# Performance work log

Hardware: AMD Instinct MI355X
Metric: run time of the kernel (lower is better)

The kernel has to match this reference:

```python
import jax, jax.numpy as jnp
import numpy as np

B, L, C, H, MAX_K, TAU = 64, 512, 256, 8, 512, 1.0
N = B * L
DH = C // H


def setup_inputs() -> dict:
    key = jax.random.key(0)
    ks = jax.random.split(key, 16)
    s = 0.02
    return {
        "x": jax.random.normal(ks[0], (N, C), jnp.float32),
        "edge_index": jax.random.randint(ks[1], (2, 200000), 0, N, jnp.int64),
        "batch": jnp.repeat(jnp.arange(B, dtype=jnp.int64), L),
        "token_ratio": jax.random.uniform(ks[2], (B,), jnp.float32, 0.05, 0.95),
        # gumbel = -log(Exp(1)) matches -empty.exponential_().log()
        "gumbel": -jnp.log(jax.random.exponential(ks[3], (B, L), jnp.float32)),
        # scorer: Linear(C,C) -> ReLU -> Linear(C,1)
        "Ws1": jax.random.normal(ks[4], (C, C), jnp.float32) * s,
        "bs1": jnp.zeros((C,), jnp.float32),
        "Ws2": jax.random.normal(ks[5], (1, C), jnp.float32) * s,
        "bs2": jnp.zeros((1,), jnp.float32),
        # MultiheadAttention packed in-proj [3C, C] and out-proj [C, C]
        "Win": jax.random.normal(ks[6], (3 * C, C), jnp.float32) * s,
        "b_in": jnp.zeros((3 * C,), jnp.float32),
        "Wout": jax.random.normal(ks[7], (C, C), jnp.float32) * s,
        "bout": jnp.zeros((C,), jnp.float32),
        # MLP: Linear(C, 2C) -> ReLU -> Linear(2C, C)
        "Wm1": jax.random.normal(ks[8], (2 * C, C), jnp.float32) * s,
        "bm1": jnp.zeros((2 * C,), jnp.float32),
        "Wm2": jax.random.normal(ks[9], (C, 2 * C), jnp.float32) * s,
        "bm2": jnp.zeros((C,), jnp.float32),
    }


def reference(x, edge_index, batch, token_ratio, gumbel,
              Ws1, bs1, Ws2, bs2, Win, b_in, Wout, bout, Wm1, bm1, Wm2, bm2):
    # conv=None, norm=None, eval mode (dropout = identity), equal-length graphs
    h_dense = x.reshape(B, L, C)                                  # to_dense_batch
    real_len = L                                                  # all graphs full
    k_per = jnp.clip(jnp.ceil(token_ratio * real_len).astype(jnp.int32),
                     1, min(MAX_K, L))                            # [B]
    k_max = int(np.max(np.asarray(k_per)))                        # concrete

    # scorer -> log-softmax scores (mask is all True, no -inf fill needed)
    s1 = jax.nn.relu(h_dense @ Ws1.T + bs1)
    scores = (s1 @ Ws2.T + bs2)[..., 0]                           # [B, L]
    log_scores = jax.nn.log_softmax(scores, axis=-1)

    # gumbel top-k with straight-through one-hot mask
    y_soft = jax.nn.softmax((log_scores + gumbel) / TAU, axis=-1)
    _, idx_g = jax.lax.top_k(y_soft, k_max)                       # [B, k_max]
    bidx = jnp.arange(B)[:, None]
    y_hard = jnp.zeros_like(y_soft).at[bidx, idx_g].set(1.0)
    token_mask = y_hard + y_soft - jax.lax.stop_gradient(y_soft)  # == y_hard numerically

    # sort descending, zero tokens beyond k_per[i], scatter back to node order
    sort_idx = jnp.argsort(-jax.lax.stop_gradient(token_mask), axis=-1, stable=True)
    sorted_mask = jnp.take_along_axis(token_mask, sort_idx, axis=1)
    keep = jnp.arange(L)[None, :] < k_per[:, None]
    sorted_mask = jnp.where(keep, sorted_mask, 0.0)
    refined = jnp.zeros_like(sorted_mask).at[bidx, sort_idx].set(sorted_mask)

    # compact gather + padded self-attention
    weighted = h_dense * refined[..., None]                       # [B, L, C]
    _, topk_idx = jax.lax.top_k(jax.lax.stop_gradient(refined), k_max)
    h_compact = jnp.take_along_axis(weighted, topk_idx[..., None], axis=1)  # [B,k,C]
    compact_mask = jnp.arange(k_max)[None, :] < k_per[:, None]    # [B, k]

    qkv = h_compact @ Win.T + b_in
    q, k, v = jnp.split(qkv, 3, axis=-1)
    hd = lambda t: t.reshape(B, k_max, H, DH)
    att = jnp.einsum('bqhd,bkhd->bhqk', hd(q), hd(k)) / np.sqrt(DH)
    att = jnp.where(compact_mask[:, None, None, :], att, -jnp.inf)
    att = jax.nn.softmax(att, axis=-1)
    h_attn = jnp.einsum('bhqk,bkhd->bqhd', att, hd(v)).reshape(B, k_max, C)
    h_attn = h_attn @ Wout.T + bout

    # scatter back to dense node positions
    h_full = jnp.zeros((B, L, C), x.dtype).at[bidx, topk_idx].set(h_attn)
    h = h_full.reshape(N, C) + x
    h = h * token_ratio[batch][:, None]

    out = h  # hs == [h] since conv is None
    out = out + (jax.nn.relu(out @ Wm1.T + bm1) @ Wm2.T + bm2)
    return out
```

## Files before the change

kernel.cpp:

```cpp
#include <hip/hip_runtime.h>
#include <hip/hip_bf16.h>
#include <math.h>

#define BB 64
#define LL 512
#define CC 256
#define HH 8
#define DHH 32
#define NN (BB * LL)

typedef __attribute__((ext_vector_type(8))) short bf16x8;
typedef __attribute__((ext_vector_type(4))) float f32x4;
typedef __attribute__((ext_vector_type(4))) unsigned short us4;

#define MFMA16(a, b, c) __builtin_amdgcn_mfma_f32_16x16x32_bf16(a, b, c, 0, 0, 0)

__device__ __forceinline__ unsigned short f2bf(float f) {
  unsigned u = __builtin_bit_cast(unsigned, f);
  u += 0x7fffu + ((u >> 16) & 1u);
  return (unsigned short)(u >> 16);
}
__device__ __forceinline__ float bf2f(unsigned short h) {
  unsigned u = ((unsigned)h) << 16;
  return __builtin_bit_cast(float, u);
}

__global__ __launch_bounds__(256) void k_cvt(
    const float* __restrict__ Ws1, unsigned short* __restrict__ W1h,
    unsigned short* __restrict__ W1l, const float* __restrict__ Win,
    unsigned short* __restrict__ Winh, const float* __restrict__ Wout,
    unsigned short* __restrict__ Wouth, const float* __restrict__ Wm1,
    unsigned short* __restrict__ Wm1h, const float* __restrict__ Wm2,
    unsigned short* __restrict__ Wm2h) {
  const int NW1 = CC * CC;
  const int NWIN = 3 * CC * CC;
  const int NWM = 2 * CC * CC;
  int i = blockIdx.x * 256 + threadIdx.x;
  if (i < NW1) {
    float v = Ws1[i];
    unsigned short hb = f2bf(v);
    W1h[i] = hb;
    W1l[i] = f2bf(v - bf2f(hb));
    return;
  }
  i -= NW1;
  if (i < NWIN) { Winh[i] = f2bf(Win[i]); return; }
  i -= NWIN;
  if (i < NW1) { Wouth[i] = f2bf(Wout[i]); return; }
  i -= NW1;
  if (i < NWM) { Wm1h[i] = f2bf(Wm1[i]); return; }
  i -= NWM;
  if (i < NWM) Wm2h[i] = f2bf(Wm2[i]);
}

__global__ __launch_bounds__(512, 4) void k_scorer(
    const float* __restrict__ x, unsigned short* __restrict__ xh,
    const unsigned short* __restrict__ W1h,
    const unsigned short* __restrict__ W1l, const float* __restrict__ bs1,
    const float* __restrict__ Ws2, const float* __restrict__ bs2,
    float* __restrict__ scores) {
  __shared__ unsigned short Ah[64][264];
  __shared__ unsigned short Al[64][264];
  __shared__ float red[8][64];
  int t = threadIdx.x;
  int tok0 = blockIdx.x * 64;
  int lane = t & 63, wid = t >> 6, quad = lane >> 4, l16 = lane & 15;
  bf16x8 bhc[2], blc[2];
#pragma unroll
  for (int nt = 0; nt < 2; ++nt) {
    int n = wid * 32 + nt * 16 + l16;
    bhc[nt] = *(const bf16x8*)&W1h[(size_t)n * CC + quad * 8];
    blc[nt] = *(const bf16x8*)&W1l[(size_t)n * CC + quad * 8];
  }
  for (int idx = t; idx < 64 * 64; idx += 512) {
    int r = idx >> 6, c4 = idx & 63;
    float4 v = *(const float4*)(x + (size_t)(tok0 + r) * CC + c4 * 4);
    float vv[4] = {v.x, v.y, v.z, v.w};
    unsigned short hb[4], lb[4];
#pragma unroll
    for (int j = 0; j < 4; ++j) {
      hb[j] = f2bf(vv[j]);
      lb[j] = f2bf(vv[j] - bf2f(hb[j]));
    }
    *(us4*)&Ah[r][c4 * 4] = *(us4*)hb;
    *(us4*)&Al[r][c4 * 4] = *(us4*)lb;
    ((us4*)(xh + (size_t)(tok0 + r) * CC))[c4] = *(us4*)hb;
  }
  __syncthreads();
  f32x4 acc[4][2] = {};
  for (int k0 = 0; k0 < CC; k0 += 32) {
    bf16x8 bhn[2], bln[2];
    bool more = (k0 + 32 < CC);
    if (more) {
#pragma unroll
      for (int nt = 0; nt < 2; ++nt) {
        int n = wid * 32 + nt * 16 + l16;
        bhn[nt] = *(const bf16x8*)&W1h[(size_t)n * CC + (k0 + 32) + quad * 8];
        bln[nt] = *(const bf16x8*)&W1l[(size_t)n * CC + (k0 + 32) + quad * 8];
      }
    }
    bf16x8 ah_[4], al_[4];
#pragma unroll
    for (int rt = 0; rt < 4; ++rt) {
      ah_[rt] = *(const bf16x8*)&Ah[rt * 16 + l16][k0 + quad * 8];
      al_[rt] = *(const bf16x8*)&Al[rt * 16 + l16][k0 + quad * 8];
    }
#pragma unroll
    for (int nt = 0; nt < 2; ++nt)
#pragma unroll
      for (int rt = 0; rt < 4; ++rt) {
        acc[rt][nt] = MFMA16(ah_[rt], bhc[nt], acc[rt][nt]);
        acc[rt][nt] = MFMA16(ah_[rt], blc[nt], acc[rt][nt]);
        acc[rt][nt] = MFMA16(al_[rt], bhc[nt], acc[rt][nt]);
      }
    if (more) {
#pragma unroll
      for (int nt = 0; nt < 2; ++nt) { bhc[nt] = bhn[nt]; blc[nt] = bln[nt]; }
    }
  }
  float rs[4][4] = {};
#pragma unroll
  for (int nt = 0; nt < 2; ++nt) {
    int n = wid * 32 + nt * 16 + l16;
    float b1 = bs1[n], w2 = Ws2[n];
#pragma unroll
    for (int rt = 0; rt < 4; ++rt)
#pragma unroll
      for (int r = 0; r < 4; ++r)
        rs[rt][r] += fmaxf(acc[rt][nt][r] + b1, 0.f) * w2;
  }
#pragma unroll
  for (int o = 1; o < 16; o <<= 1)
#pragma unroll
    for (int rt = 0; rt < 4; ++rt)
#pragma unroll
      for (int r = 0; r < 4; ++r) rs[rt][r] += __shfl_xor(rs[rt][r], o);
  if (l16 == 0) {
#pragma unroll
    for (int rt = 0; rt < 4; ++rt)
#pragma unroll
      for (int r = 0; r < 4; ++r)
        red[wid][rt * 16 + quad * 4 + r] = rs[rt][r];
  }
  __syncthreads();
  if (t < 64) {
    float s = bs2[0];
#pragma unroll
    for (int w = 0; w < 8; ++w) s += red[w][t];
    scores[tok0 + t] = s;
  }
}

__global__ __launch_bounds__(512) void k_presel(
    const float* __restrict__ scores, const float* __restrict__ gumbel,
    const float* __restrict__ ratio, int* __restrict__ k_per,
    int* __restrict__ codes, int* __restrict__ row2l) {
  __shared__ float zs[LL];
  __shared__ int sel[LL];
  __shared__ float red[8];
  __shared__ int kps[64];
  int b = blockIdx.x, l = threadIdx.x;
  int lane = l & 63, wid = l >> 6;
  if (l < 64) {
    int kp_ = (int)ceilf(ratio[l] * (float)LL);
    kp_ = min(max(kp_, 1), LL);
    kps[l] = kp_;
    if (l == b) k_per[b] = kp_;
  }
  __syncthreads();
  int kp = kps[b];
  int km = 0;
#pragma unroll
  for (int j = 0; j < 64; ++j) km = max(km, kps[j]);
  float v = scores[b * LL + l];
  float m = v;
  for (int o = 32; o > 0; o >>= 1) m = fmaxf(m, __shfl_down(m, o));
  if (lane == 0) red[wid] = m;
  __syncthreads();
  m = red[0];
#pragma unroll
  for (int j = 1; j < 8; ++j) m = fmaxf(m, red[j]);
  __syncthreads();
  float e = expf(v - m);
  for (int o = 32; o > 0; o >>= 1) e += __shfl_down(e, o);
  if (lane == 0) red[wid] = e;
  __syncthreads();
  float tot = red[0];
#pragma unroll
  for (int j = 1; j < 8; ++j) tot += red[j];
  float lse = m + logf(tot);
  float zl = v - lse + gumbel[b * LL + l];
  zs[l] = zl;
  __syncthreads();
  int rank = 0;
  for (int j = 0; j < LL; ++j) {
    float zj = zs[j];
    rank += (zj > zl) || (zj == zl && j < l);
  }
  int s = (rank < km) ? 1 : 0;
  sel[l] = s;
  __syncthreads();
  int ps = 0;
  for (int j = 0; j < l; ++j) ps += sel[j];
  int kept = s && (ps < kp);
  int keptPrefix = min(ps, kp);
  int code;
  if (kept)
    code = ps;
  else if ((l - keptPrefix) < (km - kp))
    code = kp;
  else
    code = -1;
  codes[b * LL + l] = code;
  if (kept) row2l[b * LL + ps] = l;
}

__global__ __launch_bounds__(256) void k_qkv(
    const unsigned short* __restrict__ xh, const int* __restrict__ row2l,
    const int* __restrict__ k_per, const unsigned short* __restrict__ Winh,
    const float* __restrict__ b_in, unsigned short* __restrict__ qh,
    unsigned short* __restrict__ kh, unsigned short* __restrict__ vh) {
  int b = blockIdx.y;
  int kp = k_per[b];
  int rows = (kp < LL) ? kp + 1 : LL;
  int r0 = blockIdx.x * 32;
  if (r0 >= rows) return;
  __shared__ unsigned short A1[32][264];
  int t = threadIdx.x;
  for (int idx = t; idx < 32 * 64; idx += 256) {
    int r = idx >> 6, c4 = idx & 63;
    int gr = r0 + r;
    us4 v = {0, 0, 0, 0};
    if (gr < kp) {
      int l = row2l[b * LL + gr];
      v = ((const us4*)(xh + ((size_t)b * LL + l) * CC))[c4];
    }
    *(us4*)&A1[r][c4 * 4] = v;
  }
  __syncthreads();
  int lane = t & 63, wid = t >> 6, quad = lane >> 4, row16 = lane & 15;
  f32x4 acc[2][12] = {};
  for (int k0 = 0; k0 < CC; k0 += 32) {
    bf16x8 a0 = *(const bf16x8*)&A1[row16][k0 + quad * 8];
    bf16x8 a1 = *(const bf16x8*)&A1[16 + row16][k0 + quad * 8];
#pragma unroll
    for (int nt = 0; nt < 12; ++nt) {
      int n = wid * 192 + nt * 16 + row16;
      bf16x8 bfr = *(const bf16x8*)&Winh[(size_t)n * CC + k0 + quad * 8];
      acc[0][nt] = MFMA16(a0, bfr, acc[0][nt]);
      acc[1][nt] = MFMA16(a1, bfr, acc[1][nt]);
    }
  }
#pragma unroll
  for (int rt = 0; rt < 2; ++rt) {
#pragma unroll
    for (int nt = 0; nt < 12; ++nt) {
      int n = wid * 192 + nt * 16 + row16;
      int which = n >> 8, nc = n & 255;
      unsigned short* dst = (which == 0) ? qh : (which == 1) ? kh : vh;
      float bias = b_in[n];
#pragma unroll
      for (int r = 0; r < 4; ++r) {
        int row = r0 + rt * 16 + quad * 4 + r;
        if (row < rows)
          dst[((size_t)b * LL + row) * CC + nc] = f2bf(acc[rt][nt][r] + bias);
      }
    }
  }
}

__global__ __launch_bounds__(256, 4) void k_attn(
    const unsigned short* __restrict__ qh, const unsigned short* __restrict__ kh,
    const unsigned short* __restrict__ vh, const int* __restrict__ k_per,
    unsigned short* __restrict__ ah) {
  int h = blockIdx.y, b = blockIdx.z;
  int kp = k_per[b];
  int rows = (kp < LL) ? kp + 1 : LL;
  int q0 = blockIdx.x * 128;
  if (q0 >= rows) return;
  int t = threadIdx.x;
  int lane = t & 63, wid = t >> 6, quad = lane >> 4, l16 = lane & 15;

  __shared__ unsigned short Kc[128 * 40];
  __shared__ unsigned short Vt[32 * 132];
  __shared__ unsigned short Pb[4][16 * 132];

  size_t base = ((size_t)b * LL) * CC + (size_t)h * DHH;

  bf16x8 aQ[2] = {};
  float m[2][4];
  f32x4 o0[2] = {}, o1[2] = {}, o2[2] = {};
#pragma unroll
  for (int g = 0; g < 2; ++g) {
    int myq = q0 + wid * 32 + g * 16 + l16;
    if (myq < rows)
      aQ[g] = *(const bf16x8*)(qh + base + (size_t)myq * CC + quad * 8);
#pragma unroll
    for (int r = 0; r < 4; ++r) m[g][r] = -1e30f;
  }
  bf16x8 vone;
#pragma unroll
  for (int j = 0; j < 8; ++j) vone[j] = (short)0x3F80;

  const float scale = 0.17677669529663687f;
  int nch = (kp + 127) >> 7;
  unsigned short* Pw = Pb[wid];

  int kK0 = t >> 2;
  int kc8 = (t & 3) * 8;
  int vd0 = (t & 7) * 4;
  int vk0 = (t >> 3) * 4;

  bf16x8 Kreg[2];
  us4 Vreg[4];
  auto LOADC = [&](int cc) {
    int kb = cc << 7;
#pragma unroll
    for (int i = 0; i < 2; ++i) {
      int gk = kb + kK0 + i * 64;
      bf16x8 z = {};
      if (gk < kp) z = *(const bf16x8*)(kh + base + (size_t)gk * CC + kc8);
      Kreg[i] = z;
    }
#pragma unroll
    for (int i = 0; i < 4; ++i) {
      int gk = kb + vk0 + i;
      us4 z4 = {0, 0, 0, 0};
      if (gk < kp) z4 = *(const us4*)(vh + base + (size_t)gk * CC + vd0);
      Vreg[i] = z4;
    }
  };

  LOADC(0);
  for (int c = 0; c < nch; ++c) {
    int kbase = c << 7;
    __syncthreads();
    *(bf16x8*)&Kc[kK0 * 40 + kc8] = Kreg[0];
    *(bf16x8*)&Kc[(kK0 + 64) * 40 + kc8] = Kreg[1];
#pragma unroll
    for (int j = 0; j < 4; ++j) {
      us4 w = {Vreg[0][j], Vreg[1][j], Vreg[2][j], Vreg[3][j]};
      *(us4*)&Vt[(vd0 + j) * 132 + vk0] = w;
    }
    __syncthreads();
    if (c + 1 < nch) LOADC(c + 1);
#pragma unroll
    for (int g = 0; g < 2; ++g) {
      f32x4 s[8];
      __builtin_amdgcn_s_setprio(1);
#pragma unroll
      for (int tt = 0; tt < 8; ++tt) {
        f32x4 z4 = {};
        bf16x8 bK = *(const bf16x8*)&Kc[(tt * 16 + l16) * 40 + quad * 8];
        s[tt] = MFMA16(aQ[g], bK, z4);
      }
      __builtin_amdgcn_s_setprio(0);
      float cm[4] = {-1e30f, -1e30f, -1e30f, -1e30f};
#pragma unroll
      for (int tt = 0; tt < 8; ++tt) {
        float sb = (kbase + tt * 16 + l16 < kp) ? 0.f : -1e30f;
#pragma unroll
        for (int r = 0; r < 4; ++r) {
          float v = fmaf(s[tt][r], scale, sb);
          s[tt][r] = v;
          cm[r] = fmaxf(cm[r], v);
        }
      }
#pragma unroll
      for (int o = 1; o < 16; o <<= 1)
#pragma unroll
        for (int r = 0; r < 4; ++r) cm[r] = fmaxf(cm[r], __shfl_xor(cm[r], o));
      float alpha[4];
#pragma unroll
      for (int r = 0; r < 4; ++r) {
        float mn = fmaxf(m[g][r], cm[r]);
        alpha[r] = __expf(m[g][r] - mn);
        m[g][r] = mn;
      }
#pragma unroll
      for (int tt = 0; tt < 8; ++tt)
#pragma unroll
        for (int r = 0; r < 4; ++r) s[tt][r] = __expf(s[tt][r] - m[g][r]);
#pragma unroll
      for (int r = 0; r < 4; ++r) {
        o0[g][r] *= alpha[r];
        o1[g][r] *= alpha[r];
        o2[g][r] *= alpha[r];
      }
#pragma unroll
      for (int tt = 0; tt < 8; ++tt)
#pragma unroll
        for (int r = 0; r < 4; ++r)
          Pw[(quad * 4 + r) * 132 + tt * 16 + l16] = f2bf(s[tt][r]);
      __builtin_amdgcn_s_setprio(1);
#pragma unroll
      for (int gg = 0; gg < 4; ++gg) {
        if (kbase + gg * 32 < kp) {
          bf16x8 aP = *(const bf16x8*)&Pw[l16 * 132 + gg * 32 + quad * 8];
          int koff = gg * 32 + quad * 8;
          struct U8 { us4 a, bq; };
          U8 u0, u1;
          u0.a = *(const us4*)&Vt[l16 * 132 + koff];
          u0.bq = *(const us4*)&Vt[l16 * 132 + koff + 4];
          u1.a = *(const us4*)&Vt[(16 + l16) * 132 + koff];
          u1.bq = *(const us4*)&Vt[(16 + l16) * 132 + koff + 4];
          o0[g] = MFMA16(aP, __builtin_bit_cast(bf16x8, u0), o0[g]);
          o1[g] = MFMA16(aP, __builtin_bit_cast(bf16x8, u1), o1[g]);
          o2[g] = MFMA16(aP, vone, o2[g]);
        }
      }
      __builtin_amdgcn_s_setprio(0);
    }
  }
#pragma unroll
  for (int g = 0; g < 2; ++g)
#pragma unroll
    for (int r = 0; r < 4; ++r) {
      int q = q0 + wid * 32 + g * 16 + quad * 4 + r;
      if (q < rows) {
        float invl = 1.f / o2[g][r];
        ah[base + (size_t)q * CC + l16] = f2bf(o0[g][r] * invl);
        ah[base + (size_t)q * CC + 16 + l16] = f2bf(o1[g][r] * invl);
      }
    }
}

__global__ __launch_bounds__(512, 4) void k_opmlp(
    const unsigned short* __restrict__ ah, const int* __restrict__ codes,
    const unsigned short* __restrict__ Wouth, const float* __restrict__ bout,
    const unsigned short* __restrict__ xh, const float* __restrict__ ratio,
    const unsigned short* __restrict__ Wm1h, const float* __restrict__ bm1,
    const unsigned short* __restrict__ Wm2h, const float* __restrict__ bm2,
    float* __restrict__ out) {
  int b = blockIdx.y;
  int l0 = blockIdx.x * 64;
  int t = threadIdx.x;
  __shared__ unsigned short A1[64][264];
  __shared__ unsigned short Hs[64][264];
  __shared__ int cd[64];
  if (t < 64) cd[t] = codes[b * LL + l0 + t];
  __syncthreads();
  for (int idx = t; idx < 64 * 64; idx += 512) {
    int r = idx >> 6, c4 = idx & 63;
    int c = cd[r];
    us4 v = {0, 0, 0, 0};
    if (c >= 0) v = ((const us4*)(ah + ((size_t)b * LL + c) * CC))[c4];
    *(us4*)&A1[r][c4 * 4] = v;
  }
  int lane = t & 63, wid = t >> 6, quad = lane >> 4, l16 = lane & 15;
  bf16x8 bcur[2];
#pragma unroll
  for (int nt = 0; nt < 2; ++nt)
    bcur[nt] =
        *(const bf16x8*)&Wouth[(size_t)(wid * 32 + nt * 16 + l16) * CC + quad * 8];
  unsigned short xv[4][2][4];
#pragma unroll
  for (int rt = 0; rt < 4; ++rt)
#pragma unroll
    for (int nt = 0; nt < 2; ++nt) {
      int n = wid * 32 + nt * 16 + l16;
#pragma unroll
      for (int r = 0; r < 4; ++r)
        xv[rt][nt][r] =
            xh[((size_t)b * LL + l0 + rt * 16 + quad * 4 + r) * CC + n];
    }
  __syncthreads();

  f32x4 acc[4][2] = {};
  for (int k0 = 0; k0 < CC; k0 += 32) {
    bf16x8 bnxt[2];
    bool more = (k0 + 32 < CC);
    if (more) {
#pragma unroll
      for (int nt = 0; nt < 2; ++nt)
        bnxt[nt] = *(const bf16x8*)&Wouth[(size_t)(wid * 32 + nt * 16 + l16) * CC +
                                          (k0 + 32) + quad * 8];
    }
    bf16x8 a_[4];
#pragma unroll
    for (int rt = 0; rt < 4; ++rt)
      a_[rt] = *(const bf16x8*)&A1[rt * 16 + l16][k0 + quad * 8];
#pragma unroll
    for (int nt = 0; nt < 2; ++nt)
#pragma unroll
      for (int rt = 0; rt < 4; ++rt)
        acc[rt][nt] = MFMA16(a_[rt], bcur[nt], acc[rt][nt]);
    if (more) { bcur[0] = bnxt[0]; bcur[1] = bnxt[1]; }
  }
  float rt_ratio = ratio[b];
  f32x4 acc2[4][2];
#pragma unroll
  for (int rt = 0; rt < 4; ++rt)
#pragma unroll
    for (int nt = 0; nt < 2; ++nt) {
      int n = wid * 32 + nt * 16 + l16;
      float bias = bout[n];
#pragma unroll
      for (int r = 0; r < 4; ++r) {
        int rl = rt * 16 + quad * 4 + r;
        int c = cd[rl];
        float y = (c >= 0) ? (acc[rt][nt][r] + bias) : 0.f;
        acc2[rt][nt][r] = (y + bf2f(xv[rt][nt][r])) * rt_ratio;
      }
    }
  __syncthreads();
#pragma unroll
  for (int rt = 0; rt < 4; ++rt)
#pragma unroll
    for (int nt = 0; nt < 2; ++nt) {
      int n = wid * 32 + nt * 16 + l16;
#pragma unroll
      for (int r = 0; r < 4; ++r)
        A1[rt * 16 + quad * 4 + r][n] = f2bf(acc2[rt][nt][r]);
    }
  __syncthreads();

#pragma unroll
  for (int half = 0; half < 2; ++half) {
    f32x4 acc1[4][2] = {};
    bf16x8 c1[2];
#pragma unroll
    for (int nt = 0; nt < 2; ++nt)
      c1[nt] = *(const bf16x8*)&Wm1h[(size_t)(half * 256 + wid * 32 + nt * 16 +
                                              l16) * CC + quad * 8];
    for (int k0 = 0; k0 < CC; k0 += 32) {
      bf16x8 n1[2];
      bool more = (k0 + 32 < CC);
      if (more) {
#pragma unroll
        for (int nt = 0; nt < 2; ++nt)
          n1[nt] = *(const bf16x8*)&Wm1h[(size_t)(half * 256 + wid * 32 +
                                                  nt * 16 + l16) * CC +
                                         (k0 + 32) + quad * 8];
      }
      bf16x8 a_[4];
#pragma unroll
      for (int rt = 0; rt < 4; ++rt)
        a_[rt] = *(const bf16x8*)&A1[rt * 16 + l16][k0 + quad * 8];
#pragma unroll
      for (int nt = 0; nt < 2; ++nt)
#pragma unroll
        for (int rt = 0; rt < 4; ++rt)
          acc1[rt][nt] = MFMA16(a_[rt], c1[nt], acc1[rt][nt]);
      if (more) { c1[0] = n1[0]; c1[1] = n1[1]; }
    }
    if (half == 1) __syncthreads();
#pragma unroll
    for (int rt = 0; rt < 4; ++rt)
#pragma unroll
      for (int nt = 0; nt < 2; ++nt) {
        int hc = wid * 32 + nt * 16 + l16;
        float bias = bm1[half * 256 + hc];
#pragma unroll
        for (int r = 0; r < 4; ++r) {
          float v = fmaxf(acc1[rt][nt][r] + bias, 0.f);
          Hs[rt * 16 + quad * 4 + r][hc] = f2bf(v);
        }
      }
    bf16x8 c2[2];
#pragma unroll
    for (int nt = 0; nt < 2; ++nt)
      c2[nt] = *(const bf16x8*)&Wm2h[(size_t)(wid * 32 + nt * 16 + l16) *
                                         (2 * CC) + half * 256 + quad * 8];
    __syncthreads();
    for (int k0 = 0; k0 < CC; k0 += 32) {
      bf16x8 n2[2];
      bool more = (k0 + 32 < CC);
      if (more) {
#pragma unroll
        for (int nt = 0; nt < 2; ++nt)
          n2[nt] = *(const bf16x8*)&Wm2h[(size_t)(wid * 32 + nt * 16 + l16) *
                                             (2 * CC) + half * 256 + (k0 + 32) +
                                         quad * 8];
      }
      bf16x8 h_[4];
#pragma unroll
      for (int rt = 0; rt < 4; ++rt)
        h_[rt] = *(const bf16x8*)&Hs[rt * 16 + l16][k0 + quad * 8];
#pragma unroll
      for (int nt = 0; nt < 2; ++nt)
#pragma unroll
        for (int rt = 0; rt < 4; ++rt)
          acc2[rt][nt] = MFMA16(h_[rt], c2[nt], acc2[rt][nt]);
      if (more) { c2[0] = n2[0]; c2[1] = n2[1]; }
    }
  }
#pragma unroll
  for (int rt = 0; rt < 4; ++rt)
#pragma unroll
    for (int nt = 0; nt < 2; ++nt) {
      int n = wid * 32 + nt * 16 + l16;
      float bias = bm2[n];
#pragma unroll
      for (int r = 0; r < 4; ++r) {
        int rl = rt * 16 + quad * 4 + r;
        size_t o = ((size_t)b * LL + l0 + rl) * CC + n;
        out[o] = acc2[rt][nt][r] + bias;
      }
    }
}

extern "C" void kernel_launch(void* const* d_in, const int* in_sizes, int n_in,
                              void* d_out, int out_size, void* d_ws,
                              size_t ws_size, hipStream_t stream) {
  (void)in_sizes; (void)n_in; (void)out_size; (void)ws_size;
  const float* x     = (const float*)d_in[0];
  const float* ratio = (const float*)d_in[3];
  const float* gum   = (const float*)d_in[4];
  const float* Ws1   = (const float*)d_in[5];
  const float* bs1   = (const float*)d_in[6];
  const float* Ws2   = (const float*)d_in[7];
  const float* bs2   = (const float*)d_in[8];
  const float* Win   = (const float*)d_in[9];
  const float* b_in  = (const float*)d_in[10];
  const float* Wout  = (const float*)d_in[11];
  const float* bout  = (const float*)d_in[12];
  const float* Wm1   = (const float*)d_in[13];
  const float* bm1   = (const float*)d_in[14];
  const float* Wm2   = (const float*)d_in[15];
  const float* bm2   = (const float*)d_in[16];
  float* out = (float*)d_out;

  const size_t NXC = (size_t)NN * CC;
  float* z    = (float*)d_ws;
  int* k_per  = (int*)(z + NN);
  int* codes  = k_per + 128;
  int* row2l  = codes + NN;
  unsigned short* xh    = (unsigned short*)(row2l + NN);
  unsigned short* qh    = xh + NXC;
  unsigned short* kh    = qh + NXC;
  unsigned short* vh    = kh + NXC;
  unsigned short* ahb   = vh + NXC;
  unsigned short* Winh  = ahb + NXC;
  unsigned short* Wouth = Winh + 3 * CC * CC;
  unsigned short* Wm1h  = Wouth + CC * CC;
  unsigned short* Wm2h  = Wm1h + 2 * CC * CC;
  unsigned short* W1h   = Wm2h + 2 * CC * CC;
  unsigned short* W1l   = W1h + CC * CC;

  const int cvt_total = 9 * CC * CC;
  k_cvt<<<(cvt_total + 255) / 256, 256, 0, stream>>>(
      Ws1, W1h, W1l, Win, Winh, Wout, Wouth, Wm1, Wm1h, Wm2, Wm2h);

  k_scorer<<<NN / 64, 512, 0, stream>>>(x, xh, W1h, W1l, bs1, Ws2, bs2, z);
  k_presel<<<BB, 512, 0, stream>>>(z, gum, ratio, k_per, codes, row2l);
  k_qkv<<<dim3(16, BB), 256, 0, stream>>>(xh, row2l, k_per, Winh, b_in, qh, kh, vh);
  k_attn<<<dim3(4, HH, BB), 256, 0, stream>>>(qh, kh, vh, k_per, ahb);
  k_opmlp<<<dim3(8, BB), 512, 0, stream>>>(ahb, codes, Wouth, bout, xh, ratio,
                                           Wm1h, bm1, Wm2h, bm2, out);
}
```

Before: 327.6 us.

## Compact QKV and attention grids via device-built worklists; widen QKV blocks; stage attention stores

The presel kernel now builds compacted worklists of only the needed (batch, row-chunk) tiles for the QKV and attention kernels, so those kernels stop launching many blocks that exit immediately. The QKV kernel moves to 512 threads with half the N-tiles per wave and loads its gathered rows with precomputed indices. Attention output is staged through LDS and written as 16-byte vector stores instead of scattered 2-byte stores. The cost is a small serial loop in block 0 of presel and an extra LDS round trip in the attention epilogue.

```diff
diff --git a/kernel.cpp b/kernel.cpp
--- a/kernel.cpp
+++ b/kernel.cpp
@@ -154,11 +154,14 @@
 __global__ __launch_bounds__(512) void k_presel(
     const float* __restrict__ scores, const float* __restrict__ gumbel,
     const float* __restrict__ ratio, int* __restrict__ k_per,
-    int* __restrict__ codes, int* __restrict__ row2l) {
+    int* __restrict__ codes, int* __restrict__ row2l,
+    int* __restrict__ qkv_wl, int* __restrict__ qkv_cnt,
+    int* __restrict__ atn_wl, int* __restrict__ atn_cnt) {
   __shared__ float zs[LL];
   __shared__ int sel[LL];
   __shared__ float red[8];
   __shared__ int kps[64];
+  __shared__ int offq[65], offa[65];
   int b = blockIdx.x, l = threadIdx.x;
   int lane = l & 63, wid = l >> 6;
   if (l < 64) {
@@ -168,6 +171,26 @@
     if (l == b) k_per[b] = kp_;
   }
   __syncthreads();
+  if (b == 0) {
+    if (l == 0) {
+      int oq = 0, oa = 0;
+      for (int j = 0; j < 64; ++j) {
+        int rj = (kps[j] < LL) ? kps[j] + 1 : LL;
+        offq[j] = oq; offa[j] = oa;
+        oq += (rj + 31) >> 5;
+        oa += (rj + 127) >> 7;
+      }
+      offq[64] = oq; offa[64] = oa;
+      qkv_cnt[0] = oq; atn_cnt[0] = oa;
+    }
+    __syncthreads();
+    for (int j = 0; j < 64; ++j) {
+      int nq = offq[j + 1] - offq[j];
+      int na = offa[j + 1] - offa[j];
+      if (l < nq) qkv_wl[offq[j] + l] = j * 16 + l;
+      if (l < na) atn_wl[offa[j] + l] = j * 4 + l;
+    }
+  }
   int kp = kps[b];
   int km = 0;
 #pragma unroll
@@ -215,37 +238,46 @@
   if (kept) row2l[b * LL + ps] = l;
 }
 
-__global__ __launch_bounds__(256) void k_qkv(
+__global__ __launch_bounds__(512, 4) void k_qkv(
     const unsigned short* __restrict__ xh, const int* __restrict__ row2l,
     const int* __restrict__ k_per, const unsigned short* __restrict__ Winh,
     const float* __restrict__ b_in, unsigned short* __restrict__ qh,
-    unsigned short* __restrict__ kh, unsigned short* __restrict__ vh) {
-  int b = blockIdx.y;
+    unsigned short* __restrict__ kh, unsigned short* __restrict__ vh,
+    const int* __restrict__ qkv_wl, const int* __restrict__ qkv_cnt) {
+  int bid = blockIdx.x;
+  if (bid >= qkv_cnt[0]) return;
+  int wl = qkv_wl[bid];
+  int b = wl >> 4, xchunk = wl & 15;
   int kp = k_per[b];
   int rows = (kp < LL) ? kp + 1 : LL;
-  int r0 = blockIdx.x * 32;
-  if (r0 >= rows) return;
+  int r0 = xchunk * 32;
   __shared__ unsigned short A1[32][264];
   int t = threadIdx.x;
-  for (int idx = t; idx < 32 * 64; idx += 256) {
-    int r = idx >> 6, c4 = idx & 63;
-    int gr = r0 + r;
+  int lane = t & 63, wid = t >> 6, quad = lane >> 4, row16 = lane & 15;
+
+  int c4 = t & 63, rr = t >> 6;
+  int rl[4];
+#pragma unroll
+  for (int i = 0; i < 4; ++i) {
+    int gr = r0 + rr + i * 8;
+    rl[i] = (gr < kp) ? row2l[b * LL + gr] : -1;
+  }
+#pragma unroll
+  for (int i = 0; i < 4; ++i) {
     us4 v = {0, 0, 0, 0};
-    if (gr < kp) {
-      int l = row2l[b * LL + gr];
-      v = ((const us4*)(xh + ((size_t)b * LL + l) * CC))[c4];
-    }
-    *(us4*)&A1[r][c4 * 4] = v;
-  }
-  __syncthreads();
-  int lane = t & 63, wid = t >> 6, quad = lane >> 4, row16 = lane & 15;
-  f32x4 acc[2][12] = {};
+    if (rl[i] >= 0)
+      v = ((const us4*)(xh + ((size_t)b * LL + rl[i]) * CC))[c4];
+    *(us4*)&A1[rr + i * 8][c4 * 4] = v;
+  }
+  __syncthreads();
+
+  f32x4 acc[2][6] = {};
   for (int k0 = 0; k0 < CC; k0 += 32) {
     bf16x8 a0 = *(const bf16x8*)&A1[row16][k0 + quad * 8];
     bf16x8 a1 = *(const bf16x8*)&A1[16 + row16][k0 + quad * 8];
 #pragma unroll
-    for (int nt = 0; nt < 12; ++nt) {
-      int n = wid * 192 + nt * 16 + row16;
+    for (int nt = 0; nt < 6; ++nt) {
+      int n = wid * 96 + nt * 16 + row16;
       bf16x8 bfr = *(const bf16x8*)&Winh[(size_t)n * CC + k0 + quad * 8];
       acc[0][nt] = MFMA16(a0, bfr, acc[0][nt]);
       acc[1][nt] = MFMA16(a1, bfr, acc[1][nt]);
@@ -254,8 +286,8 @@
 #pragma unroll
   for (int rt = 0; rt < 2; ++rt) {
 #pragma unroll
-    for (int nt = 0; nt < 12; ++nt) {
-      int n = wid * 192 + nt * 16 + row16;
+    for (int nt = 0; nt < 6; ++nt) {
+      int n = wid * 96 + nt * 16 + row16;
       int which = n >> 8, nc = n & 255;
       unsigned short* dst = (which == 0) ? qh : (which == 1) ? kh : vh;
       float bias = b_in[n];
@@ -272,12 +304,16 @@
 __global__ __launch_bounds__(256, 4) void k_attn(
     const unsigned short* __restrict__ qh, const unsigned short* __restrict__ kh,
     const unsigned short* __restrict__ vh, const int* __restrict__ k_per,
-    unsigned short* __restrict__ ah) {
-  int h = blockIdx.y, b = blockIdx.z;
+    unsigned short* __restrict__ ah,
+    const int* __restrict__ atn_wl, const int* __restrict__ atn_cnt) {
+  int bid = blockIdx.x;
+  if (bid >= atn_cnt[0]) return;
+  int wl = atn_wl[bid];
+  int b = wl >> 2, qi = wl & 3;
+  int h = blockIdx.y;
   int kp = k_per[b];
   int rows = (kp < LL) ? kp + 1 : LL;
-  int q0 = blockIdx.x * 128;
-  if (q0 >= rows) return;
+  int q0 = qi * 128;
   int t = threadIdx.x;
   int lane = t & 63, wid = t >> 6, quad = lane >> 4, l16 = lane & 15;
 
@@ -412,17 +448,28 @@
       __builtin_amdgcn_s_setprio(0);
     }
   }
+
+  unsigned short (*Ob)[40] = (unsigned short(*)[40]) & Pb[0][0];
+  __syncthreads();
 #pragma unroll
   for (int g = 0; g < 2; ++g)
 #pragma unroll
     for (int r = 0; r < 4; ++r) {
-      int q = q0 + wid * 32 + g * 16 + quad * 4 + r;
-      if (q < rows) {
-        float invl = 1.f / o2[g][r];
-        ah[base + (size_t)q * CC + l16] = f2bf(o0[g][r] * invl);
-        ah[base + (size_t)q * CC + 16 + l16] = f2bf(o1[g][r] * invl);
-      }
-    }
+      int ql = wid * 32 + g * 16 + quad * 4 + r;
+      float invl = 1.f / o2[g][r];
+      Ob[ql][l16] = f2bf(o0[g][r] * invl);
+      Ob[ql][16 + l16] = f2bf(o1[g][r] * invl);
+    }
+  __syncthreads();
+#pragma unroll
+  for (int i = 0; i < 2; ++i) {
+    int flat = i * 256 + t;
+    int ql = flat >> 2, c = flat & 3;
+    int q = q0 + ql;
+    if (q < rows)
+      *(bf16x8*)(ah + base + (size_t)q * CC + c * 8) =
+          *(const bf16x8*)&Ob[ql][c * 8];
+  }
 }
 
 __global__ __launch_bounds__(512, 4) void k_opmlp(
@@ -637,15 +684,22 @@
   unsigned short* Wm2h  = Wm1h + 2 * CC * CC;
   unsigned short* W1h   = Wm2h + 2 * CC * CC;
   unsigned short* W1l   = W1h + CC * CC;
+  int* qkv_wl  = (int*)(W1l + CC * CC);
+  int* qkv_cnt = qkv_wl + 1024;
+  int* atn_wl  = qkv_cnt + 1;
+  int* atn_cnt = atn_wl + 256;
 
   const int cvt_total = 9 * CC * CC;
   k_cvt<<<(cvt_total + 255) / 256, 256, 0, stream>>>(
       Ws1, W1h, W1l, Win, Winh, Wout, Wouth, Wm1, Wm1h, Wm2, Wm2h);
 
   k_scorer<<<NN / 64, 512, 0, stream>>>(x, xh, W1h, W1l, bs1, Ws2, bs2, z);
-  k_presel<<<BB, 512, 0, stream>>>(z, gum, ratio, k_per, codes, row2l);
-  k_qkv<<<dim3(16, BB), 256, 0, stream>>>(xh, row2l, k_per, Winh, b_in, qh, kh, vh);
-  k_attn<<<dim3(4, HH, BB), 256, 0, stream>>>(qh, kh, vh, k_per, ahb);
+  k_presel<<<BB, 512, 0, stream>>>(z, gum, ratio, k_per, codes, row2l,
+                                   qkv_wl, qkv_cnt, atn_wl, atn_cnt);
+  k_qkv<<<1024, 512, 0, stream>>>(xh, row2l, k_per, Winh, b_in, qh, kh, vh,
+                                  qkv_wl, qkv_cnt);
+  k_attn<<<dim3(256, HH), 256, 0, stream>>>(qh, kh, vh, k_per, ahb,
+                                            atn_wl, atn_cnt);
   k_opmlp<<<dim3(8, BB), 512, 0, stream>>>(ahb, codes, Wouth, bout, xh, ratio,
                                            Wm1h, bm1, Wm2h, bm2, out);
 }
```

Measured after the change: 316.3 us. -3.4%, faster.
